# Kernel tuning notes

Hardware: AMD Instinct MI355X
Metric: run time of the kernel (lower is better)

## Reference

```python
import jax, jax.numpy as jnp
import numpy as np

SC = np.float32(np.sqrt(0.5))


def _reflect_idx(l, m):
    # symmetric-extension gather indices for a length-l axis padded by m each side
    x = np.arange(-m, l + m, dtype=np.float64)
    minx, maxx = -0.5, l - 0.5
    rng = maxx - minx
    mod = np.fmod(x - minx, 2.0 * rng)
    mod = np.where(mod < 0, mod + 2.0 * rng, mod)
    out = np.where(mod >= rng, 2.0 * rng - mod, mod) + minx
    return out.astype(np.int32)


def _conv_h(X, h):
    # true 'valid' convolution (filter flipped, as np.convolve) along H of (N,C,H,W)
    k = h.shape[0]
    w = jnp.flip(h).reshape(1, 1, k, 1).astype(X.dtype)
    N, C, H, W = X.shape
    y = jax.lax.conv_general_dilated(X.reshape(N * C, 1, H, W), w, (1, 1), 'VALID',
                                     dimension_numbers=('NCHW', 'OIHW', 'NCHW'))
    return y.reshape(N, C, -1, W)


def colfilter(X, h):
    # odd-tap filter along rows (H) with symmetric padding, output same H
    m = h.shape[0] // 2
    xe = _reflect_idx(X.shape[2], m)
    return _conv_h(X[:, :, xe], h)


def rowfilter(X, h):
    return colfilter(X.transpose(0, 1, 3, 2), h).transpose(0, 1, 3, 2)


def colifilt(X, ha, hb, highpass):
    # Polyphase form of dtcwt's colifilt: four phase outputs interleaved into 2*H rows.
    N, C, r, W = X.shape
    m = ha.shape[0]
    m2 = m // 2
    xe = _reflect_idx(r, m2)  # len r + m
    hao, hae = ha[0::2], ha[1::2]
    hbo, hbe = hb[0::2], hb[1::2]
    if m2 % 2 == 0:
        t = np.arange(3, r + m, 2)
        off = 2
    else:
        t = np.arange(2, r + m - 1, 2)
        off = 0
    # highpass pairs have sum(ha*hb) < 0 -> swapped quarter-sample phases
    ta, tb = (t - 1, t) if highpass else (t, t - 1)
    Xb = X[:, :, xe[tb - off]]
    Xa = X[:, :, xe[ta - off]]
    Xb2 = X[:, :, xe[tb]] if off else Xb
    Xa2 = X[:, :, xe[ta]] if off else Xa
    y0 = _conv_h(Xb, hao)
    y1 = _conv_h(Xa, hbo)
    y2 = _conv_h(Xb2, hae)
    y3 = _conv_h(Xa2, hbe)
    Y = jnp.stack([y0, y1, y2, y3], axis=3)  # (N,C,r/2,4,W)
    return Y.reshape(N, C, 2 * r, W)


def rowifilt(X, ha, hb, highpass):
    return colifilt(X.transpose(0, 1, 3, 2), ha, hb, highpass).transpose(0, 1, 3, 2)


def c2q(w1, w2):
    # complex orientation pair (N,C,h,w,2) -> real quad image (N,C,2h,2w)
    w1r, w1i = w1[..., 0], w1[..., 1]
    w2r, w2i = w2[..., 0], w2[..., 1]
    x1 = (w1r + w2r) * SC  # top-left
    x2 = (w1i + w2i) * SC  # top-right
    x3 = (w1i - w2i) * SC  # bottom-left
    x4 = (w2r - w1r) * SC  # bottom-right
    N, C, H, W = x1.shape
    top = jnp.stack([x1, x2], axis=-1).reshape(N, C, H, 2 * W)
    bot = jnp.stack([x3, x4], axis=-1).reshape(N, C, H, 2 * W)
    return jnp.stack([top, bot], axis=3).reshape(N, C, 2 * H, 2 * W)


def _bands(yh):
    lh = c2q(yh[:, :, 0], yh[:, :, 5])
    hl = c2q(yh[:, :, 2], yh[:, :, 3])
    hh = c2q(yh[:, :, 1], yh[:, :, 4])
    return lh, hl, hh


def _crop(ll, ref):
    if ll.shape[2] != ref.shape[2]:
        ll = ll[:, :, 1:-1]
    if ll.shape[3] != ref.shape[3]:
        ll = ll[:, :, :, 1:-1]
    return ll


def _inv_j2plus(ll, yh, g0a, g0b, g1a, g1b):
    lh, hl, hh = _bands(yh)
    ll = _crop(ll, lh)
    y1 = colifilt(ll, g0b, g0a, False) + colifilt(lh, g1b, g1a, True)
    y2 = colifilt(hl, g0b, g0a, False) + colifilt(hh, g1b, g1a, True)
    return rowifilt(y1, g0b, g0a, False) + rowifilt(y2, g1b, g1a, True)


def _inv_j1(ll, yh, g0o, g1o):
    lh, hl, hh = _bands(yh)
    ll = _crop(ll, lh)
    y1 = colfilter(ll, g0o) + colfilter(lh, g1o)
    y2 = colfilter(hl, g0o) + colfilter(hh, g1o)
    return rowfilter(y1, g0o) + rowfilter(y2, g1o)


def _filters():
    # near_sym_a (5,7)-tap biorthogonal synthesis filters
    g0o = np.array([-3.0, -15.0, 73.0, 170.0, 73.0, -15.0, -3.0]) / 280.0
    g1o = np.array([-1.0, -5.0, 12.0, -5.0, -1.0]) / 20.0
    # qshift_06 10-tap quarter-shift filters
    h0a = np.array([0.03516384, 0.0, -0.08832942, 0.23389032, 0.76027237,
                    0.58751830, 0.0, -0.11430184, 0.0, 0.0])
    g0b = h0a
    g0a = h0a[::-1]
    g1a = h0a * np.array([1.0, -1.0] * 5)
    g1b = g1a[::-1]
    f32 = lambda a: jnp.asarray(np.ascontiguousarray(a), dtype=jnp.float32)
    return f32(g0o), f32(g1o), f32(g0a), f32(g0b), f32(g1a), f32(g1b)


def setup_inputs():
    key = jax.random.key(0)
    k1, k2, k3, k4 = jax.random.split(key, 4)
    N, C = 4, 64
    yl = jax.random.normal(k1, (N, C, 64, 64), dtype=jnp.float32)
    yh1 = jax.random.normal(k2, (N, C, 6, 128, 128, 2), dtype=jnp.float32)
    yh2 = jax.random.normal(k3, (N, C, 6, 64, 64, 2), dtype=jnp.float32)
    yh3 = jax.random.normal(k4, (N, C, 6, 32, 32, 2), dtype=jnp.float32)
    g0o, g1o, g0a, g0b, g1a, g1b = _filters()
    return {"yl": yl, "yh1": yh1, "yh2": yh2, "yh3": yh3,
            "g0o": g0o, "g1o": g1o, "g0a": g0a, "g0b": g0b, "g1a": g1a, "g1b": g1b}


def reference(yl, yh1, yh2, yh3, g0o, g1o, g0a, g0b, g1a, g1b):
    ll = _inv_j2plus(yl, yh3, g0a, g0b, g1a, g1b)   # 64 -> 128
    ll = _inv_j2plus(ll, yh2, g0a, g0b, g1a, g1b)   # 128 -> 256
    return _inv_j1(ll, yh1, g0o, g1o)               # 256 -> 256
```

## Files before the change

kernel.cpp:

```cpp
#include <hip/hip_runtime.h>

#define SC 0.70710678118654752440f

typedef _Float16 h4v __attribute__((ext_vector_type(4)));

__device__ __forceinline__ float4 ld4(const float* __restrict__ p) {
    return *(const float4*)p;
}
__device__ __forceinline__ float4 ld4(const _Float16* __restrict__ p) {
    h4v h = *(const h4v*)p;
    return make_float4((float)h[0], (float)h[1], (float)h[2], (float)h[3]);
}
__device__ __forceinline__ void st4(float* __restrict__ p, float4 v) {
    *(float4*)p = v;
}
__device__ __forceinline__ void st4(_Float16* __restrict__ p, float4 v) {
    h4v h;
    h[0] = (_Float16)v.x; h[1] = (_Float16)v.y;
    h[2] = (_Float16)v.z; h[3] = (_Float16)v.w;
    *(h4v*)p = h;
}

__device__ __forceinline__ int reflFull(int p, int n) {
    int x = max(p, ~p);
    return min(x, 2 * n - 1 - x);
}

__device__ __forceinline__ int pairRefl(int t, int NP, bool& sw) {
    int x = max(t, ~t);
    int tp = min(x, 2 * NP - 1 - x);
    sw = (tp != t);
    return tp;
}

__device__ __forceinline__ constexpr int cflIdx(int s, int k) {
    return (s == 0) ? 8 - 2 * k : (s == 1) ? 1 + 2 * k : (s == 2) ? 9 - 2 * k : 2 * k;
}
__device__ __forceinline__ constexpr int cfhIdx(int s, int k) {
    return (s == 0) ? 1 + 2 * k : (s == 1) ? 8 - 2 * k : (s == 2) ? 2 * k : 9 - 2 * k;
}

__device__ __forceinline__ float4 f4fma(float c, float4 a, float4 acc) {
    return make_float4(fmaf(c, a.x, acc.x), fmaf(c, a.y, acc.y),
                       fmaf(c, a.z, acc.z), fmaf(c, a.w, acc.w));
}
__device__ __forceinline__ float4 f4sel(bool sw, float4 a, float4 b) {
    return sw ? a : b;
}

struct Band4 { float4 e05, o05, e23, o23, e14, o14; };

__device__ __forceinline__ Band4 loadBands4(const float* __restrict__ bp, int HW2,
                                            int boff, bool sw) {
    float4 B0 = *(const float4*)(bp + 0 * HW2 + boff);
    float4 B1 = *(const float4*)(bp + 1 * HW2 + boff);
    float4 B2 = *(const float4*)(bp + 2 * HW2 + boff);
    float4 B3 = *(const float4*)(bp + 3 * HW2 + boff);
    float4 B4 = *(const float4*)(bp + 4 * HW2 + boff);
    float4 B5 = *(const float4*)(bp + 5 * HW2 + boff);
    float4 ve05 = {B0.x + B5.x, B0.y + B5.y, B0.z + B5.z, B0.w + B5.w};
    float4 vo05 = {B0.y - B5.y, B5.x - B0.x, B0.w - B5.w, B5.z - B0.z};
    float4 ve23 = {B2.x + B3.x, B2.y + B3.y, B2.z + B3.z, B2.w + B3.w};
    float4 vo23 = {B2.y - B3.y, B3.x - B2.x, B2.w - B3.w, B3.z - B2.z};
    float4 ve14 = {B1.x + B4.x, B1.y + B4.y, B1.z + B4.z, B1.w + B4.w};
    float4 vo14 = {B1.y - B4.y, B4.x - B1.x, B1.w - B4.w, B4.z - B1.z};
    Band4 r;
    r.e05 = f4sel(sw, vo05, ve05);  r.o05 = f4sel(sw, ve05, vo05);
    r.e23 = f4sel(sw, vo23, ve23);  r.o23 = f4sel(sw, ve23, vo23);
    r.e14 = f4sel(sw, vo14, ve14);  r.o14 = f4sel(sw, ve14, vo14);
    return r;
}

template <int N> struct Log2 { static constexpr int v = 1 + Log2<N / 2>::v; };
template <> struct Log2<1> { static constexpr int v = 0; };

template <int H, int W, typename TIn, typename TOut>
__global__ __launch_bounds__(256) void j2_fused(
        const TIn* __restrict__ ll, const float* __restrict__ yh,
        const float* __restrict__ g0b, const float* __restrict__ g1a,
        TOut* __restrict__ out) {
    constexpr int LOGW = Log2<W>::v;
    constexpr int U4 = W / 2, LOGU4 = LOGW - 1;
    constexpr int QI = 256 / U4;
    constexpr int TI = 4 * QI;
    constexpr int r = 2 * H, C2 = 2 * W, COUT = 4 * W, LOGC2 = LOGW + 1;
    constexpr int HW2 = H * W * 2;
    __shared__ float4 sY[TI][W];

    const int tid = threadIdx.x;
    const int nc = blockIdx.y;
    const int q0 = blockIdx.x * QI;
    const TIn* llp = ll + (size_t)nc * r * C2;
    const float* bp  = yh + (size_t)nc * 6 * HW2;

    float G0[10], G1[10];
#pragma unroll
    for (int i = 0; i < 10; ++i) { G0[i] = g0b[i]; G1[i] = g1a[i]; }

    {
        int u4 = tid & (U4 - 1);
        int qq = tid >> LOGU4;
        int q = q0 + qq;
        float4 A1[4], A1b[4], A2[4];
#pragma unroll
        for (int s = 0; s < 4; ++s) {
            A1[s] = {0, 0, 0, 0}; A1b[s] = {0, 0, 0, 0}; A2[s] = {0, 0, 0, 0};
        }
#pragma unroll
        for (int k = 0; k < 5; ++k) {
            int t = q + k - 2;
            int pe = reflFull(2 * t, r);
            int po = reflFull(2 * t + 1, r);
            float4 lle = ld4(llp + ((pe << LOGC2) + 4 * u4));
            float4 llo = ld4(llp + ((po << LOGC2) + 4 * u4));
            bool sw; int tp = pairRefl(t, H, sw);
            int boff = (tp << (LOGW + 1)) + 4 * u4;
            Band4 B = loadBands4(bp, HW2, boff, sw);
#pragma unroll
            for (int s = 0; s < 4; ++s) {
                float4 lv  = (s & 1) ? llo   : lle;
                float4 v05 = (s & 1) ? B.e05 : B.o05;
                float4 v23 = (s & 1) ? B.o23 : B.e23;
                float4 v14 = (s & 1) ? B.e14 : B.o14;
                float c0 = G0[cflIdx(s, k)];
                float c1 = G1[cfhIdx(s, k)];
                A1[s]  = f4fma(c0, lv,  A1[s]);
                A1b[s] = f4fma(c1, v05, A1b[s]);
                A2[s]  = f4fma(c0, v23, f4fma(c1, v14, A2[s]));
            }
        }
#pragma unroll
        for (int s = 0; s < 4; ++s) {
            float4 w1 = f4fma(SC, A1b[s], A1[s]);
            float4 w2 = {SC * A2[s].x, SC * A2[s].y, SC * A2[s].z, SC * A2[s].w};
            sY[4 * qq + s][2 * u4]     = make_float4(w1.x, w1.y, w2.x, w2.y);
            sY[4 * qq + s][2 * u4 + 1] = make_float4(w1.z, w1.w, w2.z, w2.w);
        }
    }
    __syncthreads();

    TOut* op = out + (size_t)nc * (4 * H) * COUT;
#pragma unroll
    for (int v = 0; v < (TI * W) / 256; ++v) {
        int lin = v * 256 + tid;
        int qc = lin & (W - 1);
        int il = lin >> LOGW;
        float e1[5], o1[5], e2[5], o2[5];
#pragma unroll
        for (int m = 0; m < 5; ++m) {
            int t = qc + m - 2;
            bool sw; int tp = pairRefl(t, W, sw);
            float4 F = sY[il][tp];
            e1[m] = sw ? F.y : F.x;  o1[m] = sw ? F.x : F.y;
            e2[m] = sw ? F.w : F.z;  o2[m] = sw ? F.z : F.w;
        }
        float acc[4];
#pragma unroll
        for (int s = 0; s < 4; ++s) {
            float a = 0.f;
#pragma unroll
            for (int k = 0; k < 5; ++k) {
                float v1 = (s & 1) ? o1[k] : e1[k];
                float v2 = (s & 1) ? e2[k] : o2[k];
                a = fmaf(G0[cflIdx(s, k)], v1, a);
                a = fmaf(G1[cfhIdx(s, k)], v2, a);
            }
            acc[s] = a;
        }
        int grow = 4 * q0 + il;
        st4(op + (size_t)grow * COUT + 4 * qc,
            make_float4(acc[0], acc[1], acc[2], acc[3]));
    }
}

template <int H, int W, typename TIn>
__global__ __launch_bounds__(256) void j1_fused(
        const TIn* __restrict__ ll, const float* __restrict__ yh,
        const float* __restrict__ g0o, const float* __restrict__ g1o,
        float* __restrict__ out) {
    constexpr int LOGW = Log2<W>::v;
    constexpr int U4 = W / 2, LOGU4 = LOGW - 1;
    constexpr int QI = 256 / U4;
    constexpr int TI = 4 * QI;
    constexpr int r = 2 * H, c = 2 * W, LOGC2 = LOGW + 1;
    constexpr int HW2 = H * W * 2;
    __shared__ float4 sY[TI][W];

    const int tid = threadIdx.x;
    const int nc = blockIdx.y;
    const int qi0 = blockIdx.x * QI;
    const TIn* llp = ll + (size_t)nc * r * c;
    const float* bp  = yh + (size_t)nc * 6 * HW2;

    float g0f[7], g1f[5];
#pragma unroll
    for (int k = 0; k < 7; ++k) g0f[k] = g0o[6 - k];
#pragma unroll
    for (int k = 0; k < 5; ++k) g1f[k] = g1o[4 - k];

    {
        int u4 = tid & (U4 - 1);
        int qq = tid >> LOGU4;
        int qi = qi0 + qq;
        float4 A1[4], A1b[4], A2[4];
#pragma unroll
        for (int s = 0; s < 4; ++s) {
            A1[s] = {0, 0, 0, 0}; A1b[s] = {0, 0, 0, 0}; A2[s] = {0, 0, 0, 0};
        }
#pragma unroll
        for (int rr = 0; rr < 10; ++rr) {
            int p = reflFull(4 * qi - 3 + rr, r);
            float4 v = ld4(llp + ((p << LOGC2) + 4 * u4));
#pragma unroll
            for (int di = 0; di < 4; ++di) {
                int k = rr - di;
                if (k >= 0 && k <= 6) A1[di] = f4fma(g0f[k], v, A1[di]);
            }
        }
#pragma unroll
        for (int tr = 0; tr < 6; ++tr) {
            int t = 2 * qi - 2 + tr;
            bool sw; int tp = pairRefl(t, H, sw);
            int boff = (tp << (LOGW + 1)) + 4 * u4;
            Band4 B = loadBands4(bp, HW2, boff, sw);
#pragma unroll
            for (int di = 0; di < 4; ++di) {
                int k1e = 2 * tr - di - 2;
                int k1o = k1e + 1;
                int k0e = 2 * tr - di - 1;
                int k0o = k0e + 1;
                if (k1e >= 0 && k1e <= 4) {
                    A1b[di] = f4fma(g1f[k1e], B.e05, A1b[di]);
                    A2[di]  = f4fma(g1f[k1e], B.e14, A2[di]);
                }
                if (k1o >= 0 && k1o <= 4) {
                    A1b[di] = f4fma(g1f[k1o], B.o05, A1b[di]);
                    A2[di]  = f4fma(g1f[k1o], B.o14, A2[di]);
                }
                if (k0e >= 0 && k0e <= 6) A2[di] = f4fma(g0f[k0e], B.e23, A2[di]);
                if (k0o >= 0 && k0o <= 6) A2[di] = f4fma(g0f[k0o], B.o23, A2[di]);
            }
        }
#pragma unroll
        for (int di = 0; di < 4; ++di) {
            float4 w1 = f4fma(SC, A1b[di], A1[di]);
            float4 w2 = {SC * A2[di].x, SC * A2[di].y, SC * A2[di].z, SC * A2[di].w};
            sY[4 * qq + di][2 * u4]     = make_float4(w1.x, w1.y, w2.x, w2.y);
            sY[4 * qq + di][2 * u4 + 1] = make_float4(w1.z, w1.w, w2.z, w2.w);
        }
    }
    __syncthreads();

    float* op = out + (size_t)nc * r * c;
#pragma unroll
    for (int v = 0; v < (TI * (W / 2)) / 256; ++v) {
        int lin = v * 256 + tid;
        int uq = lin & (W / 2 - 1);
        int il = lin >> (LOGW - 1);
        float e1[6], o1[6], e2[6], o2[6];
#pragma unroll
        for (int m = 0; m < 6; ++m) {
            int t = 2 * uq - 2 + m;
            bool sw; int tp = pairRefl(t, W, sw);
            float4 F = sY[il][tp];
            e1[m] = sw ? F.y : F.x;  o1[m] = sw ? F.x : F.y;
            e2[m] = sw ? F.w : F.z;  o2[m] = sw ? F.z : F.w;
        }
        float acc[4];
#pragma unroll
        for (int s = 0; s < 4; ++s) {
            float a = 0.f;
#pragma unroll
            for (int k = 0; k < 7; ++k) {
                int rel = s + k + 1;
                int m = rel >> 1;
                a = fmaf(g0f[k], (rel & 1) ? o1[m] : e1[m], a);
            }
#pragma unroll
            for (int k = 0; k < 5; ++k) {
                int rel = s + k + 2;
                int m = rel >> 1;
                a = fmaf(g1f[k], (rel & 1) ? o2[m] : e2[m], a);
            }
            acc[s] = a;
        }
        int grow = 4 * qi0 + il;
        *(float4*)(op + (size_t)grow * c + 4 * uq) =
            make_float4(acc[0], acc[1], acc[2], acc[3]);
    }
}

extern "C" void kernel_launch(void* const* d_in, const int* in_sizes, int n_in,
                              void* d_out, int out_size, void* d_ws, size_t ws_size,
                              hipStream_t stream) {
    const float* yl  = (const float*)d_in[0];
    const float* yh1 = (const float*)d_in[1];
    const float* yh2 = (const float*)d_in[2];
    const float* yh3 = (const float*)d_in[3];
    const float* g0o = (const float*)d_in[4];
    const float* g1o = (const float*)d_in[5];
    const float* g0b = (const float*)d_in[7];
    const float* g1a = (const float*)d_in[8];
    float* out = (float*)d_out;

    const int NC = 256;
    char* ws = (char*)d_ws;
    _Float16* llA = (_Float16*)ws;
    _Float16* llB = (_Float16*)(ws + ((size_t)16 << 20));

    j2_fused<32, 32, float, _Float16><<<dim3(2, NC), 256, 0, stream>>>(
        yl, yh3, g0b, g1a, llA);
    j2_fused<64, 64, _Float16, _Float16><<<dim3(8, NC), 256, 0, stream>>>(
        llA, yh2, g0b, g1a, llB);
    j1_fused<128, 128, _Float16><<<dim3(16, NC), 256, 0, stream>>>(
        llB, yh1, g0o, g1o, out);
}
```

Measured before the change: 100.7 us.

## Double per-thread work, store intermediate tile as fp16, fold SC into filters

Each thread now computes two adjacent output row groups in the column pass, so the overlapping input rows and band loads are shared across them. In the row pass each thread produces eight outputs and reuses the shared-memory taps that overlap. The shared tile is stored as half precision, which halves LDS footprint and traffic, and the sqrt(0.5) scaling is folded into pre-scaled filter copies. The grid is halved to match. This trades lower occupancy and more registers per thread, plus some extra rounding in the intermediate, for less redundant load work.

```diff
diff --git a/kernel.cpp b/kernel.cpp
--- a/kernel.cpp
+++ b/kernel.cpp
@@ -19,6 +19,15 @@
     h[0] = (_Float16)v.x; h[1] = (_Float16)v.y;
     h[2] = (_Float16)v.z; h[3] = (_Float16)v.w;
     *(h4v*)p = h;
+}
+__device__ __forceinline__ h4v f2h(float4 v) {
+    h4v h;
+    h[0] = (_Float16)v.x; h[1] = (_Float16)v.y;
+    h[2] = (_Float16)v.z; h[3] = (_Float16)v.w;
+    return h;
+}
+__device__ __forceinline__ float4 h2f(h4v h) {
+    return make_float4((float)h[0], (float)h[1], (float)h[2], (float)h[3]);
 }
 
 __device__ __forceinline__ int reflFull(int p, int n) {
@@ -81,95 +90,109 @@
         TOut* __restrict__ out) {
     constexpr int LOGW = Log2<W>::v;
     constexpr int U4 = W / 2, LOGU4 = LOGW - 1;
-    constexpr int QI = 256 / U4;
-    constexpr int TI = 4 * QI;
-    constexpr int r = 2 * H, C2 = 2 * W, COUT = 4 * W, LOGC2 = LOGW + 1;
+    constexpr int P = 256 / U4;
+    constexpr int TI = 8 * P;
+    constexpr int r = 2 * H, COUT = 4 * W, LOGC2 = LOGW + 1;
     constexpr int HW2 = H * W * 2;
-    __shared__ float4 sY[TI][W];
+    __shared__ h4v sY[TI][W];
 
     const int tid = threadIdx.x;
     const int nc = blockIdx.y;
-    const int q0 = blockIdx.x * QI;
-    const TIn* llp = ll + (size_t)nc * r * C2;
+    const int q0 = blockIdx.x * (TI / 4);
+    const TIn* llp = ll + (size_t)nc * r * (2 * W);
     const float* bp  = yh + (size_t)nc * 6 * HW2;
 
-    float G0[10], G1[10];
-#pragma unroll
-    for (int i = 0; i < 10; ++i) { G0[i] = g0b[i]; G1[i] = g1a[i]; }
+    float G0[10], G1[10], SG0[10], SG1[10];
+#pragma unroll
+    for (int i = 0; i < 10; ++i) {
+        G0[i] = g0b[i]; G1[i] = g1a[i];
+        SG0[i] = SC * G0[i]; SG1[i] = SC * G1[i];
+    }
 
     {
         int u4 = tid & (U4 - 1);
-        int qq = tid >> LOGU4;
-        int q = q0 + qq;
-        float4 A1[4], A1b[4], A2[4];
-#pragma unroll
-        for (int s = 0; s < 4; ++s) {
-            A1[s] = {0, 0, 0, 0}; A1b[s] = {0, 0, 0, 0}; A2[s] = {0, 0, 0, 0};
-        }
-#pragma unroll
-        for (int k = 0; k < 5; ++k) {
-            int t = q + k - 2;
+        int pk = tid >> LOGU4;
+        int qp = q0 + 2 * pk;
+        float4 A1[2][4], A2[2][4];
+#pragma unroll
+        for (int qa = 0; qa < 2; ++qa)
+#pragma unroll
+            for (int s = 0; s < 4; ++s) { A1[qa][s] = {0,0,0,0}; A2[qa][s] = {0,0,0,0}; }
+
+#pragma unroll
+        for (int tt = 0; tt < 6; ++tt) {
+            int t = qp - 2 + tt;
             int pe = reflFull(2 * t, r);
             int po = reflFull(2 * t + 1, r);
             float4 lle = ld4(llp + ((pe << LOGC2) + 4 * u4));
             float4 llo = ld4(llp + ((po << LOGC2) + 4 * u4));
             bool sw; int tp = pairRefl(t, H, sw);
-            int boff = (tp << (LOGW + 1)) + 4 * u4;
-            Band4 B = loadBands4(bp, HW2, boff, sw);
+            Band4 B = loadBands4(bp, HW2, (tp << (LOGW + 1)) + 4 * u4, sw);
+#pragma unroll
+            for (int qa = 0; qa < 2; ++qa) {
+                int k = tt - qa;
+                if (k < 0 || k > 4) continue;
+#pragma unroll
+                for (int s = 0; s < 4; ++s) {
+                    float4 lv  = (s & 1) ? llo   : lle;
+                    float4 v05 = (s & 1) ? B.e05 : B.o05;
+                    float4 v23 = (s & 1) ? B.o23 : B.e23;
+                    float4 v14 = (s & 1) ? B.e14 : B.o14;
+                    A1[qa][s] = f4fma(G0[cflIdx(s, k)], lv,
+                                f4fma(SG1[cfhIdx(s, k)], v05, A1[qa][s]));
+                    A2[qa][s] = f4fma(SG0[cflIdx(s, k)], v23,
+                                f4fma(SG1[cfhIdx(s, k)], v14, A2[qa][s]));
+                }
+            }
+        }
+#pragma unroll
+        for (int qa = 0; qa < 2; ++qa)
 #pragma unroll
             for (int s = 0; s < 4; ++s) {
-                float4 lv  = (s & 1) ? llo   : lle;
-                float4 v05 = (s & 1) ? B.e05 : B.o05;
-                float4 v23 = (s & 1) ? B.o23 : B.e23;
-                float4 v14 = (s & 1) ? B.e14 : B.o14;
-                float c0 = G0[cflIdx(s, k)];
-                float c1 = G1[cfhIdx(s, k)];
-                A1[s]  = f4fma(c0, lv,  A1[s]);
-                A1b[s] = f4fma(c1, v05, A1b[s]);
-                A2[s]  = f4fma(c0, v23, f4fma(c1, v14, A2[s]));
-            }
-        }
-#pragma unroll
-        for (int s = 0; s < 4; ++s) {
-            float4 w1 = f4fma(SC, A1b[s], A1[s]);
-            float4 w2 = {SC * A2[s].x, SC * A2[s].y, SC * A2[s].z, SC * A2[s].w};
-            sY[4 * qq + s][2 * u4]     = make_float4(w1.x, w1.y, w2.x, w2.y);
-            sY[4 * qq + s][2 * u4 + 1] = make_float4(w1.z, w1.w, w2.z, w2.w);
-        }
+                int row = 8 * pk + 4 * qa + s;
+                float4 w1 = A1[qa][s], w2 = A2[qa][s];
+                sY[row][2 * u4]     = f2h(make_float4(w1.x, w1.y, w2.x, w2.y));
+                sY[row][2 * u4 + 1] = f2h(make_float4(w1.z, w1.w, w2.z, w2.w));
+            }
     }
     __syncthreads();
 
     TOut* op = out + (size_t)nc * (4 * H) * COUT;
 #pragma unroll
-    for (int v = 0; v < (TI * W) / 256; ++v) {
+    for (int v = 0; v < (TI * W) / 512; ++v) {
         int lin = v * 256 + tid;
-        int qc = lin & (W - 1);
-        int il = lin >> LOGW;
-        float e1[5], o1[5], e2[5], o2[5];
-#pragma unroll
-        for (int m = 0; m < 5; ++m) {
-            int t = qc + m - 2;
+        int uc = lin & (U4 - 1);
+        int il = lin >> LOGU4;
+        float e1[6], o1[6], e2[6], o2[6];
+#pragma unroll
+        for (int m = 0; m < 6; ++m) {
+            int t = 2 * uc - 2 + m;
             bool sw; int tp = pairRefl(t, W, sw);
-            float4 F = sY[il][tp];
+            float4 F = h2f(sY[il][tp]);
             e1[m] = sw ? F.y : F.x;  o1[m] = sw ? F.x : F.y;
             e2[m] = sw ? F.w : F.z;  o2[m] = sw ? F.z : F.w;
         }
-        float acc[4];
-#pragma unroll
-        for (int s = 0; s < 4; ++s) {
-            float a = 0.f;
-#pragma unroll
-            for (int k = 0; k < 5; ++k) {
-                float v1 = (s & 1) ? o1[k] : e1[k];
-                float v2 = (s & 1) ? e2[k] : o2[k];
-                a = fmaf(G0[cflIdx(s, k)], v1, a);
-                a = fmaf(G1[cfhIdx(s, k)], v2, a);
-            }
-            acc[s] = a;
-        }
+        float acc[8];
+#pragma unroll
+        for (int b = 0; b < 2; ++b)
+#pragma unroll
+            for (int s = 0; s < 4; ++s) {
+                float a = 0.f;
+#pragma unroll
+                for (int k = 0; k < 5; ++k) {
+                    int m = b + k;
+                    float v1 = (s & 1) ? o1[m] : e1[m];
+                    float v2 = (s & 1) ? e2[m] : o2[m];
+                    a = fmaf(G0[cflIdx(s, k)], v1, a);
+                    a = fmaf(G1[cfhIdx(s, k)], v2, a);
+                }
+                acc[4 * b + s] = a;
+            }
         int grow = 4 * q0 + il;
-        st4(op + (size_t)grow * COUT + 4 * qc,
+        st4(op + (size_t)grow * COUT + 8 * uc,
             make_float4(acc[0], acc[1], acc[2], acc[3]));
+        st4(op + (size_t)grow * COUT + 8 * uc + 4,
+            make_float4(acc[4], acc[5], acc[6], acc[7]));
     }
 }
 
@@ -180,113 +203,126 @@
         float* __restrict__ out) {
     constexpr int LOGW = Log2<W>::v;
     constexpr int U4 = W / 2, LOGU4 = LOGW - 1;
-    constexpr int QI = 256 / U4;
-    constexpr int TI = 4 * QI;
+    constexpr int P = 256 / U4;
+    constexpr int TI = 8 * P;
     constexpr int r = 2 * H, c = 2 * W, LOGC2 = LOGW + 1;
     constexpr int HW2 = H * W * 2;
-    __shared__ float4 sY[TI][W];
+    __shared__ h4v sY[TI][W];
 
     const int tid = threadIdx.x;
     const int nc = blockIdx.y;
-    const int qi0 = blockIdx.x * QI;
+    const int qi0 = blockIdx.x * (TI / 4);
     const TIn* llp = ll + (size_t)nc * r * c;
     const float* bp  = yh + (size_t)nc * 6 * HW2;
 
-    float g0f[7], g1f[5];
-#pragma unroll
-    for (int k = 0; k < 7; ++k) g0f[k] = g0o[6 - k];
-#pragma unroll
-    for (int k = 0; k < 5; ++k) g1f[k] = g1o[4 - k];
+    float g0f[7], g1f[5], Sg0f[7], Sg1f[5];
+#pragma unroll
+    for (int k = 0; k < 7; ++k) { g0f[k] = g0o[6 - k]; Sg0f[k] = SC * g0f[k]; }
+#pragma unroll
+    for (int k = 0; k < 5; ++k) { g1f[k] = g1o[4 - k]; Sg1f[k] = SC * g1f[k]; }
 
     {
         int u4 = tid & (U4 - 1);
-        int qq = tid >> LOGU4;
-        int qi = qi0 + qq;
-        float4 A1[4], A1b[4], A2[4];
-#pragma unroll
-        for (int s = 0; s < 4; ++s) {
-            A1[s] = {0, 0, 0, 0}; A1b[s] = {0, 0, 0, 0}; A2[s] = {0, 0, 0, 0};
-        }
-#pragma unroll
-        for (int rr = 0; rr < 10; ++rr) {
-            int p = reflFull(4 * qi - 3 + rr, r);
+        int pk = tid >> LOGU4;
+        int qp = qi0 + 2 * pk;
+        float4 A1[2][4], A2[2][4];
+#pragma unroll
+        for (int qa = 0; qa < 2; ++qa)
+#pragma unroll
+            for (int di = 0; di < 4; ++di) { A1[qa][di] = {0,0,0,0}; A2[qa][di] = {0,0,0,0}; }
+
+#pragma unroll
+        for (int rr = 0; rr < 14; ++rr) {
+            int p = reflFull(4 * qp - 3 + rr, r);
             float4 v = ld4(llp + ((p << LOGC2) + 4 * u4));
 #pragma unroll
+            for (int qa = 0; qa < 2; ++qa)
+#pragma unroll
+                for (int di = 0; di < 4; ++di) {
+                    int k = rr - 4 * qa - di;
+                    if (k >= 0 && k <= 6) A1[qa][di] = f4fma(g0f[k], v, A1[qa][di]);
+                }
+        }
+#pragma unroll
+        for (int tt = 0; tt < 8; ++tt) {
+            int t = 2 * qp - 2 + tt;
+            bool sw; int tp = pairRefl(t, H, sw);
+            Band4 B = loadBands4(bp, HW2, (tp << (LOGW + 1)) + 4 * u4, sw);
+#pragma unroll
+            for (int qa = 0; qa < 2; ++qa) {
+                int tr = tt - 2 * qa;
+                if (tr < 0 || tr > 5) continue;
+#pragma unroll
+                for (int di = 0; di < 4; ++di) {
+                    int k1e = 2 * tr - di - 2;
+                    int k1o = k1e + 1;
+                    int k0e = 2 * tr - di - 1;
+                    int k0o = k0e + 1;
+                    if (k1e >= 0 && k1e <= 4) {
+                        A1[qa][di] = f4fma(Sg1f[k1e], B.e05, A1[qa][di]);
+                        A2[qa][di] = f4fma(Sg1f[k1e], B.e14, A2[qa][di]);
+                    }
+                    if (k1o >= 0 && k1o <= 4) {
+                        A1[qa][di] = f4fma(Sg1f[k1o], B.o05, A1[qa][di]);
+                        A2[qa][di] = f4fma(Sg1f[k1o], B.o14, A2[qa][di]);
+                    }
+                    if (k0e >= 0 && k0e <= 6) A2[qa][di] = f4fma(Sg0f[k0e], B.e23, A2[qa][di]);
+                    if (k0o >= 0 && k0o <= 6) A2[qa][di] = f4fma(Sg0f[k0o], B.o23, A2[qa][di]);
+                }
+            }
+        }
+#pragma unroll
+        for (int qa = 0; qa < 2; ++qa)
+#pragma unroll
             for (int di = 0; di < 4; ++di) {
-                int k = rr - di;
-                if (k >= 0 && k <= 6) A1[di] = f4fma(g0f[k], v, A1[di]);
-            }
-        }
-#pragma unroll
-        for (int tr = 0; tr < 6; ++tr) {
-            int t = 2 * qi - 2 + tr;
-            bool sw; int tp = pairRefl(t, H, sw);
-            int boff = (tp << (LOGW + 1)) + 4 * u4;
-            Band4 B = loadBands4(bp, HW2, boff, sw);
-#pragma unroll
-            for (int di = 0; di < 4; ++di) {
-                int k1e = 2 * tr - di - 2;
-                int k1o = k1e + 1;
-                int k0e = 2 * tr - di - 1;
-                int k0o = k0e + 1;
-                if (k1e >= 0 && k1e <= 4) {
-                    A1b[di] = f4fma(g1f[k1e], B.e05, A1b[di]);
-                    A2[di]  = f4fma(g1f[k1e], B.e14, A2[di]);
-                }
-                if (k1o >= 0 && k1o <= 4) {
-                    A1b[di] = f4fma(g1f[k1o], B.o05, A1b[di]);
-                    A2[di]  = f4fma(g1f[k1o], B.o14, A2[di]);
-                }
-                if (k0e >= 0 && k0e <= 6) A2[di] = f4fma(g0f[k0e], B.e23, A2[di]);
-                if (k0o >= 0 && k0o <= 6) A2[di] = f4fma(g0f[k0o], B.o23, A2[di]);
-            }
-        }
-#pragma unroll
-        for (int di = 0; di < 4; ++di) {
-            float4 w1 = f4fma(SC, A1b[di], A1[di]);
-            float4 w2 = {SC * A2[di].x, SC * A2[di].y, SC * A2[di].z, SC * A2[di].w};
-            sY[4 * qq + di][2 * u4]     = make_float4(w1.x, w1.y, w2.x, w2.y);
-            sY[4 * qq + di][2 * u4 + 1] = make_float4(w1.z, w1.w, w2.z, w2.w);
-        }
+                int row = 8 * pk + 4 * qa + di;
+                float4 w1 = A1[qa][di], w2 = A2[qa][di];
+                sY[row][2 * u4]     = f2h(make_float4(w1.x, w1.y, w2.x, w2.y));
+                sY[row][2 * u4 + 1] = f2h(make_float4(w1.z, w1.w, w2.z, w2.w));
+            }
     }
     __syncthreads();
 
     float* op = out + (size_t)nc * r * c;
 #pragma unroll
-    for (int v = 0; v < (TI * (W / 2)) / 256; ++v) {
+    for (int v = 0; v < (TI * W) / 1024; ++v) {
         int lin = v * 256 + tid;
-        int uq = lin & (W / 2 - 1);
-        int il = lin >> (LOGW - 1);
-        float e1[6], o1[6], e2[6], o2[6];
-#pragma unroll
-        for (int m = 0; m < 6; ++m) {
-            int t = 2 * uq - 2 + m;
+        int g8 = lin & (W / 4 - 1);
+        int il = lin >> (LOGW - 2);
+        float e1[8], o1[8], e2[8], o2[8];
+#pragma unroll
+        for (int m = 0; m < 8; ++m) {
+            int t = 4 * g8 - 2 + m;
             bool sw; int tp = pairRefl(t, W, sw);
-            float4 F = sY[il][tp];
+            float4 F = h2f(sY[il][tp]);
             e1[m] = sw ? F.y : F.x;  o1[m] = sw ? F.x : F.y;
             e2[m] = sw ? F.w : F.z;  o2[m] = sw ? F.z : F.w;
         }
-        float acc[4];
-#pragma unroll
-        for (int s = 0; s < 4; ++s) {
-            float a = 0.f;
-#pragma unroll
-            for (int k = 0; k < 7; ++k) {
-                int rel = s + k + 1;
-                int m = rel >> 1;
-                a = fmaf(g0f[k], (rel & 1) ? o1[m] : e1[m], a);
-            }
-#pragma unroll
-            for (int k = 0; k < 5; ++k) {
-                int rel = s + k + 2;
-                int m = rel >> 1;
-                a = fmaf(g1f[k], (rel & 1) ? o2[m] : e2[m], a);
-            }
-            acc[s] = a;
-        }
+        float acc[8];
+#pragma unroll
+        for (int b = 0; b < 2; ++b)
+#pragma unroll
+            for (int s = 0; s < 4; ++s) {
+                float a = 0.f;
+#pragma unroll
+                for (int k = 0; k < 7; ++k) {
+                    int rel = s + k + 1;
+                    int mm = (rel >> 1) + 2 * b;
+                    a = fmaf(g0f[k], (rel & 1) ? o1[mm] : e1[mm], a);
+                }
+#pragma unroll
+                for (int k = 0; k < 5; ++k) {
+                    int rel = s + k + 2;
+                    int mm = (rel >> 1) + 2 * b;
+                    a = fmaf(g1f[k], (rel & 1) ? o2[mm] : e2[mm], a);
+                }
+                acc[4 * b + s] = a;
+            }
         int grow = 4 * qi0 + il;
-        *(float4*)(op + (size_t)grow * c + 4 * uq) =
+        *(float4*)(op + (size_t)grow * c + 8 * g8) =
             make_float4(acc[0], acc[1], acc[2], acc[3]);
+        *(float4*)(op + (size_t)grow * c + 8 * g8 + 4) =
+            make_float4(acc[4], acc[5], acc[6], acc[7]);
     }
 }
 
@@ -308,10 +344,10 @@
     _Float16* llA = (_Float16*)ws;
     _Float16* llB = (_Float16*)(ws + ((size_t)16 << 20));
 
-    j2_fused<32, 32, float, _Float16><<<dim3(2, NC), 256, 0, stream>>>(
+    j2_fused<32, 32, float, _Float16><<<dim3(1, NC), 256, 0, stream>>>(
         yl, yh3, g0b, g1a, llA);
-    j2_fused<64, 64, _Float16, _Float16><<<dim3(8, NC), 256, 0, stream>>>(
+    j2_fused<64, 64, _Float16, _Float16><<<dim3(4, NC), 256, 0, stream>>>(
         llA, yh2, g0b, g1a, llB);
-    j1_fused<128, 128, _Float16><<<dim3(16, NC), 256, 0, stream>>>(
+    j1_fused<128, 128, _Float16><<<dim3(8, NC), 256, 0, stream>>>(
         llB, yh1, g0o, g1o, out);
 }
```

Measured after the change: 118.5 us. +17.7%, slower.

## Store intermediate shared tile as fp16 and compute two output quads per thread

Applied to the files above, without the earlier changes.

The intermediate tile in shared memory is now stored as packed fp16 (8 halves per entry, padded row) instead of float4 pairs, halving LDS footprint and traffic. The second pass is restructured so each thread reads overlapping 8-half chunks and produces two float4 outputs, so neighbouring stencil taps are reused from registers and fewer LDS reads are needed per output. This trades precision in the intermediate (fp16 rounding) and more registers per thread for lower LDS usage, possibly higher occupancy and fewer shared loads.

```diff
diff --git a/kernel.cpp b/kernel.cpp
--- a/kernel.cpp
+++ b/kernel.cpp
@@ -3,6 +3,7 @@
 #define SC 0.70710678118654752440f
 
 typedef _Float16 h4v __attribute__((ext_vector_type(4)));
+typedef _Float16 h8v __attribute__((ext_vector_type(8)));
 
 __device__ __forceinline__ float4 ld4(const float* __restrict__ p) {
     return *(const float4*)p;
@@ -21,11 +22,27 @@
     *(h4v*)p = h;
 }
 
+__device__ __forceinline__ h8v pack8(float4 a, float4 b) {
+    h8v h;
+    h[0] = (_Float16)a.x; h[1] = (_Float16)a.y;
+    h[2] = (_Float16)a.z; h[3] = (_Float16)a.w;
+    h[4] = (_Float16)b.x; h[5] = (_Float16)b.y;
+    h[6] = (_Float16)b.z; h[7] = (_Float16)b.w;
+    return h;
+}
+__device__ __forceinline__ void unpack8(h8v h, bool rv, float4& y1, float4& y2) {
+    float4 p = make_float4((float)h[0], (float)h[1], (float)h[2], (float)h[3]);
+    float4 q = make_float4((float)h[4], (float)h[5], (float)h[6], (float)h[7]);
+    float4 pr = make_float4(p.w, p.z, p.y, p.x);
+    float4 qr = make_float4(q.w, q.z, q.y, q.x);
+    y1 = rv ? pr : p;
+    y2 = rv ? qr : q;
+}
+
 __device__ __forceinline__ int reflFull(int p, int n) {
     int x = max(p, ~p);
     return min(x, 2 * n - 1 - x);
 }
-
 __device__ __forceinline__ int pairRefl(int t, int NP, bool& sw) {
     int x = max(t, ~t);
     int tp = min(x, 2 * NP - 1 - x);
@@ -83,14 +100,15 @@
     constexpr int U4 = W / 2, LOGU4 = LOGW - 1;
     constexpr int QI = 256 / U4;
     constexpr int TI = 4 * QI;
-    constexpr int r = 2 * H, C2 = 2 * W, COUT = 4 * W, LOGC2 = LOGW + 1;
+    constexpr int r = 2 * H, COUT = 4 * W, LOGC2 = LOGW + 1;
     constexpr int HW2 = H * W * 2;
-    __shared__ float4 sY[TI][W];
+    constexpr int NCH = W / 2;
+    __shared__ h8v sY[TI][NCH + 1];
 
     const int tid = threadIdx.x;
     const int nc = blockIdx.y;
     const int q0 = blockIdx.x * QI;
-    const TIn* llp = ll + (size_t)nc * r * C2;
+    const TIn* llp = ll + (size_t)nc * r * (2 * W);
     const float* bp  = yh + (size_t)nc * 6 * HW2;
 
     float G0[10], G1[10];
@@ -114,8 +132,7 @@
             float4 lle = ld4(llp + ((pe << LOGC2) + 4 * u4));
             float4 llo = ld4(llp + ((po << LOGC2) + 4 * u4));
             bool sw; int tp = pairRefl(t, H, sw);
-            int boff = (tp << (LOGW + 1)) + 4 * u4;
-            Band4 B = loadBands4(bp, HW2, boff, sw);
+            Band4 B = loadBands4(bp, HW2, (tp << (LOGW + 1)) + 4 * u4, sw);
 #pragma unroll
             for (int s = 0; s < 4; ++s) {
                 float4 lv  = (s & 1) ? llo   : lle;
@@ -133,43 +150,51 @@
         for (int s = 0; s < 4; ++s) {
             float4 w1 = f4fma(SC, A1b[s], A1[s]);
             float4 w2 = {SC * A2[s].x, SC * A2[s].y, SC * A2[s].z, SC * A2[s].w};
-            sY[4 * qq + s][2 * u4]     = make_float4(w1.x, w1.y, w2.x, w2.y);
-            sY[4 * qq + s][2 * u4 + 1] = make_float4(w1.z, w1.w, w2.z, w2.w);
+            sY[4 * qq + s][u4] = pack8(w1, w2);
         }
     }
     __syncthreads();
 
     TOut* op = out + (size_t)nc * (4 * H) * COUT;
 #pragma unroll
-    for (int v = 0; v < (TI * W) / 256; ++v) {
+    for (int v = 0; v < (TI * W) / 512; ++v) {
         int lin = v * 256 + tid;
-        int qc = lin & (W - 1);
-        int il = lin >> LOGW;
-        float e1[5], o1[5], e2[5], o2[5];
-#pragma unroll
-        for (int m = 0; m < 5; ++m) {
-            int t = qc + m - 2;
-            bool sw; int tp = pairRefl(t, W, sw);
-            float4 F = sY[il][tp];
-            e1[m] = sw ? F.y : F.x;  o1[m] = sw ? F.x : F.y;
-            e2[m] = sw ? F.w : F.z;  o2[m] = sw ? F.z : F.w;
-        }
-        float acc[4];
-#pragma unroll
-        for (int s = 0; s < 4; ++s) {
-            float a = 0.f;
-#pragma unroll
-            for (int k = 0; k < 5; ++k) {
-                float v1 = (s & 1) ? o1[k] : e1[k];
-                float v2 = (s & 1) ? e2[k] : o2[k];
-                a = fmaf(G0[cflIdx(s, k)], v1, a);
-                a = fmaf(G1[cfhIdx(s, k)], v2, a);
-            }
-            acc[s] = a;
-        }
+        int uc = lin & (U4 - 1);
+        int il = lin >> LOGU4;
+        float e1[6], o1[6], e2[6], o2[6];
+#pragma unroll
+        for (int d = 0; d < 3; ++d) {
+            int a = uc - 1 + d;
+            int ac = reflFull(a, NCH);
+            bool rv = (ac != a);
+            float4 y1, y2;
+            unpack8(sY[il][ac], rv, y1, y2);
+            e1[2 * d] = y1.x;  o1[2 * d] = y1.y;
+            e1[2 * d + 1] = y1.z;  o1[2 * d + 1] = y1.w;
+            e2[2 * d] = y2.x;  o2[2 * d] = y2.y;
+            e2[2 * d + 1] = y2.z;  o2[2 * d + 1] = y2.w;
+        }
+        float acc[8];
+#pragma unroll
+        for (int b = 0; b < 2; ++b)
+#pragma unroll
+            for (int s = 0; s < 4; ++s) {
+                float a = 0.f;
+#pragma unroll
+                for (int k = 0; k < 5; ++k) {
+                    int m = b + k;
+                    float v1 = (s & 1) ? o1[m] : e1[m];
+                    float v2 = (s & 1) ? e2[m] : o2[m];
+                    a = fmaf(G0[cflIdx(s, k)], v1, a);
+                    a = fmaf(G1[cfhIdx(s, k)], v2, a);
+                }
+                acc[4 * b + s] = a;
+            }
         int grow = 4 * q0 + il;
-        st4(op + (size_t)grow * COUT + 4 * qc,
+        st4(op + (size_t)grow * COUT + 8 * uc,
             make_float4(acc[0], acc[1], acc[2], acc[3]));
+        st4(op + (size_t)grow * COUT + 8 * uc + 4,
+            make_float4(acc[4], acc[5], acc[6], acc[7]));
     }
 }
 
@@ -184,7 +209,8 @@
     constexpr int TI = 4 * QI;
     constexpr int r = 2 * H, c = 2 * W, LOGC2 = LOGW + 1;
     constexpr int HW2 = H * W * 2;
-    __shared__ float4 sY[TI][W];
+    constexpr int NCH = W / 2;
+    __shared__ h8v sY[TI][NCH + 1];
 
     const int tid = threadIdx.x;
     const int nc = blockIdx.y;
@@ -221,8 +247,7 @@
         for (int tr = 0; tr < 6; ++tr) {
             int t = 2 * qi - 2 + tr;
             bool sw; int tp = pairRefl(t, H, sw);
-            int boff = (tp << (LOGW + 1)) + 4 * u4;
-            Band4 B = loadBands4(bp, HW2, boff, sw);
+            Band4 B = loadBands4(bp, HW2, (tp << (LOGW + 1)) + 4 * u4, sw);
 #pragma unroll
             for (int di = 0; di < 4; ++di) {
                 int k1e = 2 * tr - di - 2;
@@ -245,48 +270,55 @@
         for (int di = 0; di < 4; ++di) {
             float4 w1 = f4fma(SC, A1b[di], A1[di]);
             float4 w2 = {SC * A2[di].x, SC * A2[di].y, SC * A2[di].z, SC * A2[di].w};
-            sY[4 * qq + di][2 * u4]     = make_float4(w1.x, w1.y, w2.x, w2.y);
-            sY[4 * qq + di][2 * u4 + 1] = make_float4(w1.z, w1.w, w2.z, w2.w);
+            sY[4 * qq + di][u4] = pack8(w1, w2);
         }
     }
     __syncthreads();
 
     float* op = out + (size_t)nc * r * c;
 #pragma unroll
-    for (int v = 0; v < (TI * (W / 2)) / 256; ++v) {
+    for (int v = 0; v < (TI * W) / 1024; ++v) {
         int lin = v * 256 + tid;
-        int uq = lin & (W / 2 - 1);
-        int il = lin >> (LOGW - 1);
-        float e1[6], o1[6], e2[6], o2[6];
-#pragma unroll
-        for (int m = 0; m < 6; ++m) {
-            int t = 2 * uq - 2 + m;
-            bool sw; int tp = pairRefl(t, W, sw);
-            float4 F = sY[il][tp];
-            e1[m] = sw ? F.y : F.x;  o1[m] = sw ? F.x : F.y;
-            e2[m] = sw ? F.w : F.z;  o2[m] = sw ? F.z : F.w;
-        }
-        float acc[4];
-#pragma unroll
-        for (int s = 0; s < 4; ++s) {
-            float a = 0.f;
-#pragma unroll
-            for (int k = 0; k < 7; ++k) {
-                int rel = s + k + 1;
-                int m = rel >> 1;
-                a = fmaf(g0f[k], (rel & 1) ? o1[m] : e1[m], a);
-            }
-#pragma unroll
-            for (int k = 0; k < 5; ++k) {
-                int rel = s + k + 2;
-                int m = rel >> 1;
-                a = fmaf(g1f[k], (rel & 1) ? o2[m] : e2[m], a);
-            }
-            acc[s] = a;
-        }
+        int g8 = lin & (W / 4 - 1);
+        int il = lin >> (LOGW - 2);
+        float e1[8], o1[8], e2[8], o2[8];
+#pragma unroll
+        for (int d = 0; d < 4; ++d) {
+            int a = 2 * g8 - 1 + d;
+            int ac = reflFull(a, NCH);
+            bool rv = (ac != a);
+            float4 y1, y2;
+            unpack8(sY[il][ac], rv, y1, y2);
+            e1[2 * d] = y1.x;  o1[2 * d] = y1.y;
+            e1[2 * d + 1] = y1.z;  o1[2 * d + 1] = y1.w;
+            e2[2 * d] = y2.x;  o2[2 * d] = y2.y;
+            e2[2 * d + 1] = y2.z;  o2[2 * d + 1] = y2.w;
+        }
+        float acc[8];
+#pragma unroll
+        for (int b = 0; b < 2; ++b)
+#pragma unroll
+            for (int s = 0; s < 4; ++s) {
+                float a = 0.f;
+#pragma unroll
+                for (int k = 0; k < 7; ++k) {
+                    int rel = s + k + 1;
+                    int mm = (rel >> 1) + 2 * b;
+                    a = fmaf(g0f[k], (rel & 1) ? o1[mm] : e1[mm], a);
+                }
+#pragma unroll
+                for (int k = 0; k < 5; ++k) {
+                    int rel = s + k + 2;
+                    int mm = (rel >> 1) + 2 * b;
+                    a = fmaf(g1f[k], (rel & 1) ? o2[mm] : e2[mm], a);
+                }
+                acc[4 * b + s] = a;
+            }
         int grow = 4 * qi0 + il;
-        *(float4*)(op + (size_t)grow * c + 4 * uq) =
+        *(float4*)(op + (size_t)grow * c + 8 * g8) =
             make_float4(acc[0], acc[1], acc[2], acc[3]);
+        *(float4*)(op + (size_t)grow * c + 8 * g8 + 4) =
+            make_float4(acc[4], acc[5], acc[6], acc[7]);
     }
 }
 
```

Result: no change. 100.4 us (median of 2 runs) (-0.3%).
